# Kernel optimization log

Measured on AMD Instinct MI355X. Metric: run time of the kernel, lower is better.

## Reference

```python
import jax, jax.numpy as jnp
import numpy as np

B, T, C, HS = 8, 2048, 2048, 128  # batch, seq, n_embedding, head_size
THETA = 10000.0


def _rope_tables(dim, seq_len, theta=THETA):
    freqs = 1.0 / theta ** (jnp.arange(0, dim, 2, dtype=jnp.float32) / dim)  # [dim/2]
    t = jnp.arange(seq_len, dtype=jnp.float32)
    ang = jnp.outer(t, freqs)  # [T, dim/2]
    return jnp.cos(ang), jnp.sin(ang)


def _apply_rope(v, cos, sin):
    # v: [B,T,D]; pairs along last dim treated as complex (real=even, imag=odd)
    b, t, d = v.shape
    vr = v.reshape(b, t, d // 2, 2)
    x0, x1 = vr[..., 0], vr[..., 1]
    o0 = x0 * cos - x1 * sin
    o1 = x0 * sin + x1 * cos
    return jnp.stack([o0, o1], axis=-1).reshape(b, t, d)


def setup_inputs() -> dict:
    key = jax.random.key(0)
    k1, k2, k3, k4 = jax.random.split(key, 4)
    scale = 1.0 / np.sqrt(C)
    x = jax.random.normal(k1, (B, T, C), dtype=jnp.float32)
    Wk = jax.random.normal(k2, (C, HS), dtype=jnp.float32) * scale
    Wq = jax.random.normal(k3, (C, HS), dtype=jnp.float32) * scale
    Wv = jax.random.normal(k4, (C, HS), dtype=jnp.float32) * scale
    return {"x": x, "Wk": Wk, "Wq": Wq, "Wv": Wv}


def reference(x, Wk, Wq, Wv):
    b, t, _ = x.shape
    cos, sin = _rope_tables(HS, t)
    k = x @ Wk  # [B,T,HS]
    q = x @ Wq
    # Source: xq,xk = apply_rotary_emb(key, query); query,key = xq,xk
    # => scores = rope(q_proj) @ rope(k_proj)^T (standard causal attention)
    qr = _apply_rope(q, cos, sin)
    kr = _apply_rope(k, cos, sin)
    scores = jnp.einsum('btd,bsd->bts', qr, kr) * (HS ** -0.5)  # [B,T,T]
    causal = jnp.tril(jnp.ones((t, t), dtype=bool))
    scores = jnp.where(causal, scores, -jnp.inf)
    wei = jax.nn.softmax(scores, axis=-1)
    v = x @ Wv
    return jnp.einsum('bts,bsd->btd', wei, v)
```

## Files before the change

### kernel.cpp

```cpp
#include <hip/hip_runtime.h>

#define NB 8
#define NT 2048
#define NC 2048
#define NH 128

typedef short s8v __attribute__((ext_vector_type(8)));
typedef short s4v __attribute__((ext_vector_type(4)));
typedef float f4  __attribute__((ext_vector_type(4)));

static __device__ __forceinline__ unsigned short f2bf(float f) {
    union { float f; unsigned int u; } v; v.f = f;
    unsigned int x = v.u;
    return (unsigned short)((x + 0x7FFFu + ((x >> 16) & 1u)) >> 16);
}

static __device__ __forceinline__ s8v pack8(f4 lo, f4 hi) {
    union { f4 f; unsigned int u[4]; } L, H; L.f = lo; H.f = hi;
    union { s8v s; unsigned int u[4]; } A;
    A.u[0] = __builtin_amdgcn_perm(L.u[1], L.u[0], 0x07060302u);
    A.u[1] = __builtin_amdgcn_perm(L.u[3], L.u[2], 0x07060302u);
    A.u[2] = __builtin_amdgcn_perm(H.u[1], H.u[0], 0x07060302u);
    A.u[3] = __builtin_amdgcn_perm(H.u[3], H.u[2], 0x07060302u);
    return A.s;
}

static __device__ __forceinline__ void gl2lds16(const void* g, void* lds_base) {
    __builtin_amdgcn_global_load_lds(
        (const __attribute__((address_space(1))) unsigned int*)g,
        (__attribute__((address_space(3))) unsigned int*)lds_base, 16, 0, 0);
}

__global__ __launch_bounds__(256) void wtrans_k(
    const float* __restrict__ Wk, const float* __restrict__ Wq,
    const float* __restrict__ Wv, unsigned short* __restrict__ wt)
{
    __shared__ float Ls[64][129];
    const int mat = blockIdx.y;
    const float* W = (mat == 0) ? Wq : (mat == 1) ? Wk : Wv;
    const int k0 = blockIdx.x * 64;
    const int t  = threadIdx.x;

    #pragma unroll
    for (int j = 0; j < 8; ++j) {
        int flat = j * 1024 + t * 4;
        int k = flat >> 7, n = flat & 127;
        f4 v = *reinterpret_cast<const f4*>(W + (size_t)(k0 + k) * NH + n);
        Ls[k][n] = v[0]; Ls[k][n + 1] = v[1]; Ls[k][n + 2] = v[2]; Ls[k][n + 3] = v[3];
    }
    __syncthreads();

    const int n = t >> 1, half = t & 1;
    unsigned short tmp[32];
    #pragma unroll
    for (int kk = 0; kk < 32; ++kk) tmp[kk] = f2bf(Ls[half * 32 + kk][n]);

    const int nb  = mat * 8 + (n >> 4);
    const int l16 = n & 15;
    const int kbi = blockIdx.x * 2 + half;
    unsigned short* dst = wt + ((size_t)nb * 64 + kbi) * 512;
    #pragma unroll
    for (int v = 0; v < 4; ++v)
        *reinterpret_cast<s8v*>(dst + (v * 16 + l16) * 8) = *reinterpret_cast<s8v*>(tmp + v * 8);
}

__global__ __launch_bounds__(512) void proj_rope(
    const float* __restrict__ x, const unsigned short* __restrict__ wt,
    unsigned short* __restrict__ qp, unsigned short* __restrict__ kp,
    unsigned short* __restrict__ vp)
{
    __shared__ float Xs[2][4096];

    const int tid  = threadIdx.x;
    const int wave = tid >> 6;
    const int lane = tid & 63;
    const int quad = lane >> 4, l16 = lane & 15;
    const int M0 = blockIdx.x * 64;

    const float* xsrc[2];
    #pragma unroll
    for (int s = 0; s < 2; ++s) {
        const int xrow = wave * 8 + s * 4 + (lane >> 4);
        const int xcol = ((lane & 15) ^ (xrow & 15)) * 4;
        xsrc[s] = x + (size_t)(M0 + xrow) * NC + xcol;
    }

    const unsigned short* wtb = wt + (size_t)(wave * 3) * 32768 + lane * 8;

    f4 acc[4][3];
    #pragma unroll
    for (int mi = 0; mi < 4; ++mi)
        #pragma unroll
        for (int ni = 0; ni < 3; ++ni)
            acc[mi][ni] = (f4){0.f, 0.f, 0.f, 0.f};

    #pragma unroll
    for (int s = 0; s < 2; ++s)
        gl2lds16(xsrc[s], (char*)Xs[0] + (wave * 2 + s) * 1024);
    __syncthreads();

    for (int t = 0; t < 32; ++t) {
        s8v b[2][3];
        #pragma unroll
        for (int ks = 0; ks < 2; ++ks)
            #pragma unroll
            for (int ni = 0; ni < 3; ++ni)
                b[ks][ni] = *reinterpret_cast<const s8v*>(
                    wtb + (size_t)ni * 32768 + (size_t)(t * 2 + ks) * 512);
        if (t < 31) {
            #pragma unroll
            for (int s = 0; s < 2; ++s)
                gl2lds16(xsrc[s] + (t + 1) * 64, (char*)Xs[(t + 1) & 1] + (wave * 2 + s) * 1024);
        }
        const float* cur = Xs[t & 1];
        #pragma unroll
        for (int ksub = 0; ksub < 2; ++ksub) {
            s8v a[4];
            #pragma unroll
            for (int mi = 0; mi < 4; ++mi) {
                const int rb = (mi * 16 + l16) * 64;
                const int p0 = (ksub * 8 + quad * 2) ^ l16;
                f4 L = *reinterpret_cast<const f4*>(cur + rb + p0 * 4);
                f4 H = *reinterpret_cast<const f4*>(cur + rb + (p0 ^ 1) * 4);
                a[mi] = pack8(L, H);
            }
            #pragma unroll
            for (int ni = 0; ni < 3; ++ni)
                #pragma unroll
                for (int mi = 0; mi < 4; ++mi)
                    acc[mi][ni] = __builtin_amdgcn_mfma_f32_16x16x32_bf16(a[mi], b[ksub][ni], acc[mi][ni], 0, 0, 0);
        }
        __syncthreads();
    }

    const float cfreq = -0.10381025296f;
    const int tb = M0 >> 11;
    const int tl = M0 & 2047;
    unsigned short* qpB = qp + (size_t)tb * 262144;
    unsigned short* kpB = kp + (size_t)tb * 262144;
    unsigned short* vpB = vp + (size_t)tb * 262144;
    const int kt0 = tl >> 6;

    #pragma unroll
    for (int mi = 0; mi < 4; ++mi) {
        #pragma unroll
        for (int ni = 0; ni < 3; ++ni) {
            const int outcol = wave * 48 + ni * 16 + l16;
            const int mat = outcol >> 7;
            const int col = outcol & 127;
            float vv[4];
            #pragma unroll
            for (int r = 0; r < 4; ++r) {
                const int t = tl + mi * 16 + quad * 4 + r;
                float v = acc[mi][ni][r];
                if (mat < 2) {
                    float other = __shfl_xor(v, 1, 64);
                    float freq  = exp2f(cfreq * (float)(col & ~1));
                    float ang   = (float)t * freq;
                    float sn = sinf(ang), cs = cosf(ang);
                    v = (col & 1) ? (other * sn + v * cs)
                                  : (v * cs - other * sn);
                }
                vv[r] = v;
            }
            if (mat == 0) {
                const int qt = (tl >> 5) + (mi >> 1);
                const int ks = col >> 5, qq = (col >> 3) & 3, e = col & 7;
                unsigned short* d = qpB + ((((size_t)qt * 2 + (mi & 1)) * 4 + ks) * 64 + qq * 16 + quad * 4) * 8 + e;
                #pragma unroll
                for (int r = 0; r < 4; ++r) d[r * 8] = f2bf(vv[r]);
            } else if (mat == 1) {
                const int ks = col >> 5, qq = (col >> 3) & 3, e = col & 7;
                unsigned short* d = kpB + ((((size_t)kt0 * 4 + mi) * 4 + ks) * 64 + qq * 16 + quad * 4) * 8 + e;
                #pragma unroll
                for (int r = 0; r < 4; ++r) d[r * 8] = f2bf(vv[r]);
            } else {
                const int dt  = col >> 4;
                const int ks2 = mi >> 1;
                const int qv  = (mi & 1) * 2 + (quad >> 1);
                const int e4  = (quad & 1) * 4;
                unsigned short* d = vpB + ((((size_t)kt0 * 2 + ks2) * 8 + dt) * 64 + qv * 16 + l16) * 8 + e4;
                s4v pk;
                #pragma unroll
                for (int r = 0; r < 4; ++r) pk[r] = (short)f2bf(vv[r]);
                *reinterpret_cast<s4v*>(d) = pk;
            }
        }
    }
}

__global__ __launch_bounds__(256, 2) void attn_k(
    const unsigned short* __restrict__ qp, const unsigned short* __restrict__ kp,
    const unsigned short* __restrict__ vp, float* __restrict__ out)
{
    __shared__ unsigned short P[4][32 * 64];
    __shared__ float Os[4][32][64];
    __shared__ float Ms[4][32], Ls[4][32], Lt[32];

    const int wave = threadIdx.x >> 6;
    const int lane = threadIdx.x & 63;
    const int quad = lane >> 4, l16 = lane & 15;
    const int b     = blockIdx.y;
    const int qrow0 = blockIdx.x * 32;
    const int qt    = blockIdx.x;
    const unsigned short* Qp = qp + (size_t)b * 262144;
    const unsigned short* Kp = kp + (size_t)b * 262144;
    const unsigned short* Vp = vp + (size_t)b * 262144;

    s8v qf[2][4];
    #pragma unroll
    for (int mi = 0; mi < 2; ++mi)
        #pragma unroll
        for (int ks = 0; ks < 4; ++ks)
            qf[mi][ks] = *reinterpret_cast<const s8v*>(
                Qp + ((((size_t)qt * 2 + mi) * 4 + ks) * 64 + lane) * 8);

    float m[2][4], ls[2][4];
    f4 o[2][8];
    #pragma unroll
    for (int mi = 0; mi < 2; ++mi) {
        #pragma unroll
        for (int r = 0; r < 4; ++r) { m[mi][r] = -INFINITY; ls[mi][r] = 0.f; }
        #pragma unroll
        for (int dt = 0; dt < 8; ++dt) o[mi][dt] = (f4){0.f, 0.f, 0.f, 0.f};
    }

    const int nkt = (qrow0 >> 6) + 1;
    const float scale2 = 0.1275166948f;

    for (int kt = wave; kt < nkt; kt += 4) {
        const int kbase = kt * 64;
        const bool domask = (kt == nkt - 1);
        const unsigned short* Kt = Kp + (size_t)kt * 8192;
        const unsigned short* Vt = Vp + (size_t)kt * 8192;

        f4 s[2][4];
        #pragma unroll
        for (int nt = 0; nt < 4; ++nt) {
            f4 a0 = (f4){0.f, 0.f, 0.f, 0.f}, a1 = a0;
            #pragma unroll
            for (int ks = 0; ks < 4; ++ks) {
                s8v kf = *reinterpret_cast<const s8v*>(Kt + (((nt * 4 + ks) * 64) + lane) * 8);
                a0 = __builtin_amdgcn_mfma_f32_16x16x32_bf16(qf[0][ks], kf, a0, 0, 0, 0);
                a1 = __builtin_amdgcn_mfma_f32_16x16x32_bf16(qf[1][ks], kf, a1, 0, 0, 0);
            }
            s[0][nt] = a0; s[1][nt] = a1;
        }

        float tmx[2][4];
        #pragma unroll
        for (int mi = 0; mi < 2; ++mi) {
            #pragma unroll
            for (int r = 0; r < 4; ++r) {
                const int trow = qrow0 + mi * 16 + quad * 4 + r;
                #pragma unroll
                for (int nt = 0; nt < 4; ++nt) {
                    float sv = s[mi][nt][r] * scale2;
                    if (domask && (kbase + nt * 16 + l16 > trow)) sv = -INFINITY;
                    s[mi][nt][r] = sv;
                }
                float tm = fmaxf(fmaxf(s[mi][0][r], s[mi][1][r]),
                                 fmaxf(s[mi][2][r], s[mi][3][r]));
                #pragma unroll
                for (int off = 1; off < 16; off <<= 1)
                    tm = fmaxf(tm, __shfl_xor(tm, off, 64));
                tmx[mi][r] = tm;
            }
        }

        bool grow = false;
        #pragma unroll
        for (int mi = 0; mi < 2; ++mi)
            #pragma unroll
            for (int r = 0; r < 4; ++r)
                grow = grow || (tmx[mi][r] > m[mi][r] + 8.0f);
        if (__any(grow)) {
            #pragma unroll
            for (int mi = 0; mi < 2; ++mi)
                #pragma unroll
                for (int r = 0; r < 4; ++r) {
                    const float mn = fmaxf(m[mi][r], tmx[mi][r]);
                    const float alpha = exp2f(m[mi][r] - mn);
                    m[mi][r] = mn;
                    ls[mi][r] *= alpha;
                    #pragma unroll
                    for (int dt = 0; dt < 8; ++dt) o[mi][dt][r] *= alpha;
                }
        }

        #pragma unroll
        for (int mi = 0; mi < 2; ++mi)
            #pragma unroll
            for (int r = 0; r < 4; ++r) {
                float rs = 0.f;
                #pragma unroll
                for (int nt = 0; nt < 4; ++nt) {
                    float p = exp2f(s[mi][nt][r] - m[mi][r]);
                    s[mi][nt][r] = p;
                    rs += p;
                }
                ls[mi][r] += rs;
            }

        #pragma unroll
        for (int mi = 0; mi < 2; ++mi)
            #pragma unroll
            for (int nt = 0; nt < 4; ++nt)
                #pragma unroll
                for (int r = 0; r < 4; ++r) {
                    const int prow = mi * 16 + quad * 4 + r;
                    const int swz  = ((nt * 2 + (l16 >> 3)) ^ (prow & 7)) * 8 + (l16 & 7);
                    P[wave][prow * 64 + swz] = f2bf(s[mi][nt][r]);
                }

        #pragma unroll
        for (int ks2 = 0; ks2 < 2; ++ks2) {
            s8v pa[2];
            #pragma unroll
            for (int mi = 0; mi < 2; ++mi) {
                const int prow = mi * 16 + l16;
                const int pp = ((ks2 * 4 + quad) ^ (l16 & 7));
                pa[mi] = *reinterpret_cast<const s8v*>(&P[wave][prow * 64 + pp * 8]);
            }
            #pragma unroll
            for (int dt = 0; dt < 8; ++dt) {
                s8v vf = *reinterpret_cast<const s8v*>(Vt + (((ks2 * 8 + dt) * 64) + lane) * 8);
                o[0][dt] = __builtin_amdgcn_mfma_f32_16x16x32_bf16(pa[0], vf, o[0][dt], 0, 0, 0);
                o[1][dt] = __builtin_amdgcn_mfma_f32_16x16x32_bf16(pa[1], vf, o[1][dt], 0, 0, 0);
            }
        }
    }

    #pragma unroll
    for (int mi = 0; mi < 2; ++mi)
        #pragma unroll
        for (int r = 0; r < 4; ++r) {
            float v = ls[mi][r];
            #pragma unroll
            for (int off = 1; off < 16; off <<= 1) v += __shfl_xor(v, off, 64);
            ls[mi][r] = v;
        }

    if (l16 == 0) {
        #pragma unroll
        for (int mi = 0; mi < 2; ++mi)
            #pragma unroll
            for (int r = 0; r < 4; ++r) {
                Ms[wave][mi * 16 + quad * 4 + r] = m[mi][r];
                Ls[wave][mi * 16 + quad * 4 + r] = ls[mi][r];
            }
    }
    __syncthreads();

    #pragma unroll
    for (int mi = 0; mi < 2; ++mi)
        #pragma unroll
        for (int r = 0; r < 4; ++r) {
            const int row = mi * 16 + quad * 4 + r;
            float M = fmaxf(fmaxf(Ms[0][row], Ms[1][row]), fmaxf(Ms[2][row], Ms[3][row]));
            float sc = exp2f(m[mi][r] - M);
            float lt = Ls[0][row] * exp2f(Ms[0][row] - M) + Ls[1][row] * exp2f(Ms[1][row] - M)
                     + Ls[2][row] * exp2f(Ms[2][row] - M) + Ls[3][row] * exp2f(Ms[3][row] - M);
            if (wave == 0 && l16 == 0) Lt[row] = lt;
            #pragma unroll
            for (int dt = 0; dt < 8; ++dt) o[mi][dt][r] *= sc;
        }

    const int rrow = threadIdx.x >> 3;
    const int cx   = (threadIdx.x & 7) * 8;
    #pragma unroll
    for (int h = 0; h < 2; ++h) {
        __syncthreads();
        #pragma unroll
        for (int mi = 0; mi < 2; ++mi)
            #pragma unroll
            for (int dtl = 0; dtl < 4; ++dtl)
                #pragma unroll
                for (int r = 0; r < 4; ++r)
                    Os[wave][mi * 16 + quad * 4 + r][dtl * 16 + l16] = o[mi][h * 4 + dtl][r];
        __syncthreads();
        f4 s0 = (f4){0.f, 0.f, 0.f, 0.f}, s1 = s0;
        #pragma unroll
        for (int w = 0; w < 4; ++w) {
            s0 += *reinterpret_cast<const f4*>(&Os[w][rrow][cx]);
            s1 += *reinterpret_cast<const f4*>(&Os[w][rrow][cx + 4]);
        }
        const float rl = 1.0f / Lt[rrow];
        float* dst = &out[((size_t)b * NT + qrow0 + rrow) * NH + h * 64 + cx];
        *reinterpret_cast<f4*>(dst)     = s0 * rl;
        *reinterpret_cast<f4*>(dst + 4) = s1 * rl;
    }
}

extern "C" void kernel_launch(void* const* d_in, const int* in_sizes, int n_in,
                              void* d_out, int out_size, void* d_ws, size_t ws_size,
                              hipStream_t stream) {
    const float* x  = (const float*)d_in[0];
    const float* Wk = (const float*)d_in[1];
    const float* Wq = (const float*)d_in[2];
    const float* Wv = (const float*)d_in[3];
    unsigned short* ws   = (unsigned short*)d_ws;
    unsigned short* wt   = ws;
    unsigned short* qws  = ws  + 786432;
    unsigned short* kws  = qws + 2097152;
    unsigned short* vtws = kws + 2097152;
    float* outp = (float*)d_out;

    wtrans_k<<<dim3(32, 3), 256, 0, stream>>>(Wk, Wq, Wv, wt);
    proj_rope<<<dim3(256), 512, 0, stream>>>(x, wt, qws, kws, vtws);
    attn_k<<<dim3(64, 8), 256, 0, stream>>>(qws, kws, vtws, outp);
}
```

Baseline: 295.9 us.

## Rewrite projection GEMM to load x directly into registers without LDS

The QKV projection kernel no longer stages x tiles through double-buffered shared memory with async global-to-LDS loads. Each workgroup now covers 32 rows with 4 waves, and each wave computes 6 column tiles. The A fragments are read straight from global memory into registers and converted to bf16 there. This drops the LDS traffic and the per-iteration barriers and doubles the grid to 512 blocks. In exchange, x is re-read from global/L2 by every wave with a less coalesced pattern, and each block reuses less of the weight data.

Measured after the change: 325.3 us. +9.9%, slower.

```diff
diff --git a/kernel.cpp b/kernel.cpp
--- a/kernel.cpp
+++ b/kernel.cpp
@@ -23,12 +23,6 @@
     A.u[2] = __builtin_amdgcn_perm(H.u[1], H.u[0], 0x07060302u);
     A.u[3] = __builtin_amdgcn_perm(H.u[3], H.u[2], 0x07060302u);
     return A.s;
-}
-
-static __device__ __forceinline__ void gl2lds16(const void* g, void* lds_base) {
-    __builtin_amdgcn_global_load_lds(
-        (const __attribute__((address_space(1))) unsigned int*)g,
-        (__attribute__((address_space(3))) unsigned int*)lds_base, 16, 0, 0);
 }
 
 __global__ __launch_bounds__(256) void wtrans_k(
@@ -64,88 +58,66 @@
         *reinterpret_cast<s8v*>(dst + (v * 16 + l16) * 8) = *reinterpret_cast<s8v*>(tmp + v * 8);
 }
 
-__global__ __launch_bounds__(512) void proj_rope(
+__global__ __launch_bounds__(256) void proj_rope(
     const float* __restrict__ x, const unsigned short* __restrict__ wt,
     unsigned short* __restrict__ qp, unsigned short* __restrict__ kp,
     unsigned short* __restrict__ vp)
 {
-    __shared__ float Xs[2][4096];
-
     const int tid  = threadIdx.x;
     const int wave = tid >> 6;
     const int lane = tid & 63;
     const int quad = lane >> 4, l16 = lane & 15;
-    const int M0 = blockIdx.x * 64;
-
-    const float* xsrc[2];
-    #pragma unroll
-    for (int s = 0; s < 2; ++s) {
-        const int xrow = wave * 8 + s * 4 + (lane >> 4);
-        const int xcol = ((lane & 15) ^ (xrow & 15)) * 4;
-        xsrc[s] = x + (size_t)(M0 + xrow) * NC + xcol;
-    }
-
-    const unsigned short* wtb = wt + (size_t)(wave * 3) * 32768 + lane * 8;
-
-    f4 acc[4][3];
-    #pragma unroll
-    for (int mi = 0; mi < 4; ++mi)
-        #pragma unroll
-        for (int ni = 0; ni < 3; ++ni)
+    const int M0 = blockIdx.x * 32;
+
+    const float* xb[2];
+    #pragma unroll
+    for (int mi = 0; mi < 2; ++mi)
+        xb[mi] = x + (size_t)(M0 + mi * 16 + l16) * NC + quad * 8;
+
+    const unsigned short* bb[6];
+    #pragma unroll
+    for (int ni = 0; ni < 6; ++ni)
+        bb[ni] = wt + ((size_t)(wave * 6 + ni) * 64) * 512 + lane * 8;
+
+    f4 acc[2][6];
+    #pragma unroll
+    for (int mi = 0; mi < 2; ++mi)
+        #pragma unroll
+        for (int ni = 0; ni < 6; ++ni)
             acc[mi][ni] = (f4){0.f, 0.f, 0.f, 0.f};
 
-    #pragma unroll
-    for (int s = 0; s < 2; ++s)
-        gl2lds16(xsrc[s], (char*)Xs[0] + (wave * 2 + s) * 1024);
-    __syncthreads();
-
-    for (int t = 0; t < 32; ++t) {
-        s8v b[2][3];
-        #pragma unroll
-        for (int ks = 0; ks < 2; ++ks)
-            #pragma unroll
-            for (int ni = 0; ni < 3; ++ni)
-                b[ks][ni] = *reinterpret_cast<const s8v*>(
-                    wtb + (size_t)ni * 32768 + (size_t)(t * 2 + ks) * 512);
-        if (t < 31) {
-            #pragma unroll
-            for (int s = 0; s < 2; ++s)
-                gl2lds16(xsrc[s] + (t + 1) * 64, (char*)Xs[(t + 1) & 1] + (wave * 2 + s) * 1024);
-        }
-        const float* cur = Xs[t & 1];
-        #pragma unroll
-        for (int ksub = 0; ksub < 2; ++ksub) {
-            s8v a[4];
-            #pragma unroll
-            for (int mi = 0; mi < 4; ++mi) {
-                const int rb = (mi * 16 + l16) * 64;
-                const int p0 = (ksub * 8 + quad * 2) ^ l16;
-                f4 L = *reinterpret_cast<const f4*>(cur + rb + p0 * 4);
-                f4 H = *reinterpret_cast<const f4*>(cur + rb + (p0 ^ 1) * 4);
-                a[mi] = pack8(L, H);
-            }
-            #pragma unroll
-            for (int ni = 0; ni < 3; ++ni)
-                #pragma unroll
-                for (int mi = 0; mi < 4; ++mi)
-                    acc[mi][ni] = __builtin_amdgcn_mfma_f32_16x16x32_bf16(a[mi], b[ksub][ni], acc[mi][ni], 0, 0, 0);
-        }
-        __syncthreads();
+    #pragma unroll 2
+    for (int kb = 0; kb < 64; ++kb) {
+        s8v a[2];
+        #pragma unroll
+        for (int mi = 0; mi < 2; ++mi) {
+            f4 L = *reinterpret_cast<const f4*>(xb[mi] + kb * 32);
+            f4 H = *reinterpret_cast<const f4*>(xb[mi] + kb * 32 + 4);
+            a[mi] = pack8(L, H);
+        }
+        #pragma unroll
+        for (int ni = 0; ni < 6; ++ni) {
+            s8v b = *reinterpret_cast<const s8v*>(bb[ni] + (size_t)kb * 512);
+            acc[0][ni] = __builtin_amdgcn_mfma_f32_16x16x32_bf16(a[0], b, acc[0][ni], 0, 0, 0);
+            acc[1][ni] = __builtin_amdgcn_mfma_f32_16x16x32_bf16(a[1], b, acc[1][ni], 0, 0, 0);
+        }
     }
 
     const float cfreq = -0.10381025296f;
-    const int tb = M0 >> 11;
-    const int tl = M0 & 2047;
+    const int tb   = M0 >> 11;
+    const int tl   = M0 & 2047;
+    const int half = (tl >> 5) & 1;
     unsigned short* qpB = qp + (size_t)tb * 262144;
     unsigned short* kpB = kp + (size_t)tb * 262144;
     unsigned short* vpB = vp + (size_t)tb * 262144;
+    const int qt  = tl >> 5;
     const int kt0 = tl >> 6;
 
     #pragma unroll
-    for (int mi = 0; mi < 4; ++mi) {
-        #pragma unroll
-        for (int ni = 0; ni < 3; ++ni) {
-            const int outcol = wave * 48 + ni * 16 + l16;
+    for (int mi = 0; mi < 2; ++mi) {
+        #pragma unroll
+        for (int ni = 0; ni < 6; ++ni) {
+            const int outcol = wave * 96 + ni * 16 + l16;
             const int mat = outcol >> 7;
             const int col = outcol & 127;
             float vv[4];
@@ -164,20 +136,20 @@
                 vv[r] = v;
             }
             if (mat == 0) {
-                const int qt = (tl >> 5) + (mi >> 1);
                 const int ks = col >> 5, qq = (col >> 3) & 3, e = col & 7;
-                unsigned short* d = qpB + ((((size_t)qt * 2 + (mi & 1)) * 4 + ks) * 64 + qq * 16 + quad * 4) * 8 + e;
+                unsigned short* d = qpB + ((((size_t)qt * 2 + mi) * 4 + ks) * 64 + qq * 16 + quad * 4) * 8 + e;
                 #pragma unroll
                 for (int r = 0; r < 4; ++r) d[r * 8] = f2bf(vv[r]);
             } else if (mat == 1) {
                 const int ks = col >> 5, qq = (col >> 3) & 3, e = col & 7;
-                unsigned short* d = kpB + ((((size_t)kt0 * 4 + mi) * 4 + ks) * 64 + qq * 16 + quad * 4) * 8 + e;
+                const int nt = half * 2 + mi;
+                unsigned short* d = kpB + ((((size_t)kt0 * 4 + nt) * 4 + ks) * 64 + qq * 16 + quad * 4) * 8 + e;
                 #pragma unroll
                 for (int r = 0; r < 4; ++r) d[r * 8] = f2bf(vv[r]);
             } else {
                 const int dt  = col >> 4;
-                const int ks2 = mi >> 1;
-                const int qv  = (mi & 1) * 2 + (quad >> 1);
+                const int ks2 = half;
+                const int qv  = mi * 2 + (quad >> 1);
                 const int e4  = (quad & 1) * 4;
                 unsigned short* d = vpB + ((((size_t)kt0 * 2 + ks2) * 8 + dt) * 64 + qv * 16 + l16) * 8 + e4;
                 s4v pk;
@@ -407,6 +379,6 @@
     float* outp = (float*)d_out;
 
     wtrans_k<<<dim3(32, 3), 256, 0, stream>>>(Wk, Wq, Wv, wt);
-    proj_rope<<<dim3(256), 512, 0, stream>>>(x, wt, qws, kws, vtws);
+    proj_rope<<<dim3(512), 256, 0, stream>>>(x, wt, qws, kws, vtws);
     attn_k<<<dim3(64, 8), 256, 0, stream>>>(qws, kws, vtws, outp);
 }
```
